# Kernel tuning notes

Hardware: AMD Instinct MI355X
Metric: run time of the kernel (lower is better)

Reference implementation:

```python
import jax, jax.numpy as jnp
import numpy as np

N_NODES = 2048
IN_FEAT = 128
N_HEADS = 4
N_HIDDEN = 16  # out_features // n_heads = 64 // 4
NEG_SLOPE = 0.2


def setup_inputs() -> dict:
    key = jax.random.key(0)
    k1, k2, k3, k4, k5 = jax.random.split(key, 5)
    h = jax.random.normal(k1, (N_NODES, IN_FEAT), dtype=jnp.float32)
    adj_mat = jax.random.randint(k2, (N_NODES, N_NODES, 1), 0, 2, dtype=jnp.int32)
    scale_w = 1.0 / np.sqrt(IN_FEAT)
    W_l = jax.random.normal(k3, (IN_FEAT, N_HEADS * N_HIDDEN), dtype=jnp.float32) * scale_w
    W_r = jax.random.normal(k4, (IN_FEAT, N_HEADS * N_HIDDEN), dtype=jnp.float32) * scale_w
    attn_w = jax.random.normal(k5, (N_HIDDEN,), dtype=jnp.float32) / np.sqrt(N_HIDDEN)
    return {"h": h, "adj_mat": adj_mat, "W_l": W_l, "W_r": W_r, "attn_w": attn_w}


def reference(h, adj_mat, W_l, W_r, attn_w):
    n = h.shape[0]
    g_l = (h @ W_l).reshape(n, N_HEADS, N_HIDDEN)  # source-side proj
    g_r = (h @ W_r).reshape(n, N_HEADS, N_HIDDEN)  # target-side proj
    # g_sum[i, j, h, f] = g_r[i] + g_l[j]  (matches repeat / repeat_interleave in torch)
    g_sum = g_r[:, None, :, :] + g_l[None, :, :, :]  # [N, N, H, F]
    e = jnp.einsum('ijhf,f->ijh', jax.nn.leaky_relu(g_sum, NEG_SLOPE), attn_w)
    e = jnp.where(adj_mat == 0, -jnp.inf, e)
    a = jnp.nan_to_num(jax.nn.softmax(e, axis=1))  # softmax over neighbors j
    attn_res = jnp.einsum('ijh,jhf->ihf', a, g_r)
    return attn_res.reshape(n, N_HEADS * N_HIDDEN)  # is_concat=True
```

## Files before the change

### kernel.cpp

```cpp
#include <hip/hip_runtime.h>
#include <math.h>
#include <stdint.h>

#define NN 2048
#define IF 128
#define NH 4
#define NF 16
#define OF 64
#define JS 2
#define JT 16
#define NPW 2
#define NPB 8
#define PSTR 17
#define LOG2E 1.44269504f


typedef float f32x2 __attribute__((ext_vector_type(2)));
typedef float f32x4 __attribute__((ext_vector_type(4)));

__device__ __forceinline__ float rfl(float x) {
    return __int_as_float(__builtin_amdgcn_readfirstlane(__float_as_int(x)));
}
__device__ __forceinline__ void gl2lds16(const void* g, void* l) {
    __builtin_amdgcn_global_load_lds((const __attribute__((address_space(1))) void*)g,
                                     (__attribute__((address_space(3))) void*)l, 16, 0, 0);
}
__device__ __forceinline__ void gl2lds4(const void* g, void* l) {
    __builtin_amdgcn_global_load_lds((const __attribute__((address_space(1))) void*)g,
                                     (__attribute__((address_space(3))) void*)l, 4, 0, 0);
}

__global__ __launch_bounds__(256) void pack_kernel(const int* __restrict__ adj,
                                                   uint32_t* __restrict__ bits) {
    const int w = threadIdx.x >> 6, lane = threadIdx.x & 63;
    const int i = blockIdx.x * 4 + w;
    const int* row = adj + (size_t)i * NN;
    uint64_t*  dst = (uint64_t*)bits + (size_t)i * 32;
    #pragma unroll 4
    for (int k = 0; k < 32; ++k) {
        const int v = row[k * 64 + lane];
        const uint64_t msk = __ballot(v != 0);
        if (lane == 0) dst[k] = msk;
    }
}

__global__ __launch_bounds__(256) void proj_kernel(const float* __restrict__ h,
                                                   const float* __restrict__ Wl,
                                                   const float* __restrict__ Wr,
                                                   const float* __restrict__ attn_w,
                                                   float* __restrict__ glt,
                                                   float* __restrict__ grt,
                                                   float* __restrict__ cj6,
                                                   float* __restrict__ cjB,
                                                   float* __restrict__ ai2) {
    const int t    = threadIdx.x;
    const int w    = t >> 6, lane = t & 63;
    const int il   = w >> 1, which = w & 1;
    const int i    = blockIdx.x * 2 + il;

    __shared__ float hs[2][IF];
    hs[t >> 7][t & 127] = h[(blockIdx.x * 2 + (t >> 7)) * IF + (t & 127)];
    __syncthreads();

    const float* W = which ? Wr : Wl;
    float acc = 0.f;
    #pragma unroll
    for (int k = 0; k < IF; ++k)
        acc = fmaf(hs[il][k], W[k * OF + lane], acc);

    float* g = which ? grt : glt;
    g[(lane >> 4) * (NN * NF) + i * NF + (lane & 15)] = acc;

    const float awv = attn_w[lane & 15];
    float v  = acc * awv;
    float vb = fabsf(acc) * fabsf(awv);
    #pragma unroll
    for (int off = 1; off <= 8; off <<= 1) {
        v  += __shfl_xor(v,  off);
        vb += __shfl_xor(vb, off);
    }
    if ((lane & 15) == 0) {
        const int hh = lane >> 4;
        if (which) {
            ai2[hh * NN + i] = 0.4f * LOG2E * vb;
        } else {
            const float c2 = 0.6f * LOG2E * v;
            cj6[hh * NN + i] = c2;
            cjB[hh * NN + i] = fmaf(0.4f * LOG2E, vb, c2);
        }
    }
}

__global__ __launch_bounds__(256) void mh_kernel(const float* __restrict__ cjB,
                                                 float* __restrict__ mh) {
    const int hh = blockIdx.x, t = threadIdx.x;
    float mx = -INFINITY;
    for (int j = t; j < NN; j += 256) mx = fmaxf(mx, cjB[hh * NN + j]);
    #pragma unroll
    for (int off = 32; off; off >>= 1) mx = fmaxf(mx, __shfl_xor(mx, off));
    __shared__ float wmx[4];
    if ((t & 63) == 0) wmx[t >> 6] = mx;
    __syncthreads();
    if (t == 0) mh[hh] = fmaxf(fmaxf(wmx[0], wmx[1]), fmaxf(wmx[2], wmx[3]));
}

__global__ __launch_bounds__(256) __attribute__((amdgpu_waves_per_eu(2, 8)))
void gat_kernel(const float* __restrict__ glt,
                const float* __restrict__ grt,
                const float* __restrict__ cj6,
                const float* __restrict__ ai2,
                const float* __restrict__ mh,
                const uint32_t* __restrict__ bits,
                const float* __restrict__ attn_w,
                float* __restrict__ part) {
    const int t    = threadIdx.x;
    const int wid  = t >> 6, lane = t & 63;
    const int h    = blockIdx.x & 3;
    const int grp  = (blockIdx.x >> 2) & 255;
    const int s    = blockIdx.x >> 10;

    __shared__ __attribute__((aligned(16))) char smem[17920];
    float*    tile   = (float*)smem;
    uint32_t* bits_s = (uint32_t*)(smem + 16384);
    float*    c_s    = (float*)(smem + 17408);

    {
        const int idx = wid * 64 + lane;
        gl2lds4(bits + ((size_t)(grp * 8 + (idx >> 5))) * 64 + s * 32 + (idx & 31),
                smem + 16384 + wid * 256);
    }

    float aw_s[NF];
    #pragma unroll
    for (int f = 0; f < NF; ++f) aw_s[f] = rfl(attn_w[f]) * (0.4f * LOG2E);
    const float mh_s = rfl(mh[h]);
    float gi_s[NPW][NF], cni[NPW];
    #pragma unroll
    for (int n = 0; n < NPW; ++n) {
        const int i_n = grp * NPB + wid * NPW + n;
        #pragma unroll
        for (int f = 0; f < NF; ++f)
            gi_s[n][f] = rfl(grt[h * (NN * NF) + i_n * NF + f]);
        cni[n] = -(rfl(ai2[h * NN + i_n]) + mh_s);
    }

    const float* glh = glt + (size_t)h * NN * NF + (size_t)s * JT * 64 * NF;
    const float* grh = grt + (size_t)h * NN * NF + (size_t)s * JT * 64 * NF;
    const float* cjh = cj6 + h * NN + s * (JT * 64);

    const int soff = (wid * 16 + (lane >> 2)) * NF + (((lane & 3) ^ ((lane >> 3) & 3)) << 2);

#define STAGE(tl, nb)                                                              \
    {                                                                              \
        gl2lds16(glh + (size_t)(tl) * (64 * NF) + soff, smem + (nb) * 4096 + wid * 1024);        \
        gl2lds16(grh + (size_t)(tl) * (64 * NF) + soff, smem + 8192 + (nb) * 4096 + wid * 1024); \
        if (wid == 0) gl2lds4(cjh + (tl) * 64 + lane, smem + 17408 + (nb) * 256);  \
    }

    float l[NPW];
    f32x2 acc[NPW][8];
    #pragma unroll
    for (int n = 0; n < NPW; ++n) {
        l[n] = 0.f;
        #pragma unroll
        for (int k = 0; k < 8; ++k) acc[n][k] = (f32x2){0.f, 0.f};
    }

    STAGE(0, 0);
    __syncthreads();

    const int sh   = lane & 31;
    const int csw  = (lane >> 1) & 3;
    #pragma unroll 2
    for (int tt = 0; tt < JT; ++tt) {
        const int buf = tt & 1;
        if (tt + 1 < JT) STAGE(tt + 1, buf ^ 1);

        float ss[NPW] = {0.f, 0.f};
        #pragma unroll
        for (int q = 0; q < 4; ++q) {
            const int c = q ^ csw;
            const f32x4 gv = *(const f32x4*)&tile[buf * 1024 + lane * NF + c * 4];
            #pragma unroll
            for (int n = 0; n < NPW; ++n) {
                ss[n] = fmaf(fabsf(gv[0] + gi_s[n][q * 4 + 0]), aw_s[q * 4 + 0], ss[n]);
                ss[n] = fmaf(fabsf(gv[1] + gi_s[n][q * 4 + 1]), aw_s[q * 4 + 1], ss[n]);
                ss[n] = fmaf(fabsf(gv[2] + gi_s[n][q * 4 + 2]), aw_s[q * 4 + 2], ss[n]);
                ss[n] = fmaf(fabsf(gv[3] + gi_s[n][q * 4 + 3]), aw_s[q * 4 + 3], ss[n]);
            }
        }
        const float cj = c_s[buf * 64 + lane];

        float p[NPW];
        #pragma unroll
        for (int n = 0; n < NPW; ++n) {
            const uint32_t wb = bits_s[(wid * NPW + n) * 32 + tt * 2 + (lane >> 5)];
            const bool  kk = ((wb >> sh) & 1u) != 0u;
            float e = (ss[n] + cj) + cni[n];
            e = kk ? e : -INFINITY;
            const float pp = __builtin_amdgcn_exp2f(e);
            l[n] += pp;
            p[n] = pp;
        }

        #pragma unroll
        for (int q = 0; q < 4; ++q) {
            const int c = q ^ csw;
            const f32x4 rv = *(const f32x4*)&tile[2048 + buf * 1024 + lane * NF + c * 4];
            const f32x2 lo = {rv[0], rv[1]};
            const f32x2 hi = {rv[2], rv[3]};
            #pragma unroll
            for (int n = 0; n < NPW; ++n) {
                const f32x2 pp2 = {p[n], p[n]};
                acc[n][q * 2 + 0] = __builtin_elementwise_fma(pp2, lo, acc[n][q * 2 + 0]);
                acc[n][q * 2 + 1] = __builtin_elementwise_fma(pp2, hi, acc[n][q * 2 + 1]);
            }
        }
        __syncthreads();
    }
#undef STAGE

    float (*red)[16][PSTR] = (float (*)[16][PSTR])smem;
    #pragma unroll
    for (int n = 0; n < NPW; ++n) {
        float L = l[n];
        #pragma unroll
        for (int off = 32; off; off >>= 1) L += __shfl_xor(L, off);

        #pragma unroll
        for (int f = 0; f < NF; ++f) {
            float a = acc[n][f >> 1][f & 1];
            a += __shfl_xor(a, 32);
            a += __shfl_xor(a, 16);
            if (lane < 16) red[wid][lane][f] = a;
        }
        const int i_n = grp * NPB + wid * NPW + n;
        float* P = part + ((size_t)s * NH * NN + (size_t)h * NN + i_n) * PSTR;
        if (lane < NF) {
            float a = 0.f;
            #pragma unroll
            for (int r = 0; r < 16; ++r) a += red[wid][r][lane];
            P[lane] = a;
        } else if (lane == 16) P[16] = L;
    }
}

__global__ __launch_bounds__(256) void reduce_kernel(const float* __restrict__ part,
                                                     float* __restrict__ out) {
    const int c  = blockIdx.x * 256 + threadIdx.x;
    const int f  = c & 15;
    const int ih = c >> 4;
    float L = 0.f, a = 0.f;
    #pragma unroll
    for (int ss = 0; ss < JS; ++ss) {
        const float* P = part + ((size_t)ss * NH * NN + ih) * PSTR;
        a += P[f];
        L += P[16];
    }
    const float o = (L > 0.f) ? a / L : 0.f;
    const int i = ih & (NN - 1);
    const int h = ih >> 11;
    out[(size_t)i * OF + h * NF + f] = o;
}

extern "C" void kernel_launch(void* const* d_in, const int* in_sizes, int n_in,
                              void* d_out, int out_size, void* d_ws, size_t ws_size,
                              hipStream_t stream) {
    const float* h      = (const float*)d_in[0];
    const int*   adj    = (const int*)d_in[1];
    const float* W_l    = (const float*)d_in[2];
    const float* W_r    = (const float*)d_in[3];
    const float* attn_w = (const float*)d_in[4];
    float*       out    = (float*)d_out;

    float*    glt  = (float*)d_ws;
    float*    grt  = glt + (size_t)NN * OF;
    float*    cj6  = grt + (size_t)NN * OF;
    float*    cjB  = cj6 + (size_t)NH * NN;
    float*    ai2  = cjB + (size_t)NH * NN;
    float*    mh   = ai2 + (size_t)NH * NN;
    uint32_t* bits = (uint32_t*)(mh + 64);
    float*    prt  = (float*)(bits + (size_t)NN * 64);

    pack_kernel<<<NN / 4, 256, 0, stream>>>(adj, bits);
    proj_kernel<<<NN / 2, 256, 0, stream>>>(h, W_l, W_r, attn_w, glt, grt, cj6, cjB, ai2);
    mh_kernel<<<NH, 256, 0, stream>>>(cjB, mh);
    gat_kernel<<<JS * 256 * NH, 256, 0, stream>>>(glt, grt, cj6, ai2, mh, bits, attn_w, prt);
    reduce_kernel<<<NH * NN * NF / 256, 256, 0, stream>>>(prt, out);
}
```

Measured before the change: 60.74 us.

## Load j-tiles directly into registers and double node count per wave

The attention kernel stops staging gl/gr tiles through LDS with a barrier per tile. Each lane now loads its own j-row straight from global memory into registers, double-buffered across two steps. Each wave also handles 4 target nodes instead of 2, so every loaded j-row is reused more and the grid shrinks to half as many blocks. The cost is much higher register pressure (waves_per_eu capped at 3), lower occupancy and fewer blocks to spread latency hiding.

```diff
diff --git a/kernel.cpp b/kernel.cpp
--- a/kernel.cpp
+++ b/kernel.cpp
@@ -9,21 +9,16 @@
 #define OF 64
 #define JS 2
 #define JT 16
-#define NPW 2
-#define NPB 8
+#define NPW 4
+#define NPB 16
 #define PSTR 17
 #define LOG2E 1.44269504f
 
-
 typedef float f32x2 __attribute__((ext_vector_type(2)));
 typedef float f32x4 __attribute__((ext_vector_type(4)));
 
 __device__ __forceinline__ float rfl(float x) {
     return __int_as_float(__builtin_amdgcn_readfirstlane(__float_as_int(x)));
-}
-__device__ __forceinline__ void gl2lds16(const void* g, void* l) {
-    __builtin_amdgcn_global_load_lds((const __attribute__((address_space(1))) void*)g,
-                                     (__attribute__((address_space(3))) void*)l, 16, 0, 0);
 }
 __device__ __forceinline__ void gl2lds4(const void* g, void* l) {
     __builtin_amdgcn_global_load_lds((const __attribute__((address_space(1))) void*)g,
@@ -104,7 +99,7 @@
     if (t == 0) mh[hh] = fmaxf(fmaxf(wmx[0], wmx[1]), fmaxf(wmx[2], wmx[3]));
 }
 
-__global__ __launch_bounds__(256) __attribute__((amdgpu_waves_per_eu(2, 8)))
+__global__ __launch_bounds__(256) __attribute__((amdgpu_waves_per_eu(2, 3)))
 void gat_kernel(const float* __restrict__ glt,
                 const float* __restrict__ grt,
                 const float* __restrict__ cj6,
@@ -116,18 +111,25 @@
     const int t    = threadIdx.x;
     const int wid  = t >> 6, lane = t & 63;
     const int h    = blockIdx.x & 3;
-    const int grp  = (blockIdx.x >> 2) & 255;
-    const int s    = blockIdx.x >> 10;
-
-    __shared__ __attribute__((aligned(16))) char smem[17920];
-    float*    tile   = (float*)smem;
-    uint32_t* bits_s = (uint32_t*)(smem + 16384);
-    float*    c_s    = (float*)(smem + 17408);
-
+    const int grp  = (blockIdx.x >> 2) & 127;
+    const int s    = blockIdx.x >> 9;
+
+    __shared__ uint32_t bits_s[NPB * 32];
+    __shared__ float    c_all[JT * 64];
+    __shared__ float    red[4][16][PSTR];
+
+    #pragma unroll
+    for (int k = 0; k < 2; ++k) {
+        const int f = wid * 128 + k * 64 + lane;
+        gl2lds4(bits + ((size_t)(grp * 16 + (f >> 5))) * 64 + s * 32 + (f & 31),
+                (char*)bits_s + (wid * 128 + k * 64) * 4);
+    }
     {
-        const int idx = wid * 64 + lane;
-        gl2lds4(bits + ((size_t)(grp * 8 + (idx >> 5))) * 64 + s * 32 + (idx & 31),
-                smem + 16384 + wid * 256);
+        const float* cjh = cj6 + h * NN + s * (JT * 64);
+        #pragma unroll
+        for (int k = 0; k < 4; ++k)
+            gl2lds4(cjh + k * 256 + wid * 64 + lane,
+                    (char*)c_all + (k * 256 + wid * 64) * 4);
     }
 
     float aw_s[NF];
@@ -144,17 +146,60 @@
         cni[n] = -(rfl(ai2[h * NN + i_n]) + mh_s);
     }
 
-    const float* glh = glt + (size_t)h * NN * NF + (size_t)s * JT * 64 * NF;
-    const float* grh = grt + (size_t)h * NN * NF + (size_t)s * JT * 64 * NF;
-    const float* cjh = cj6 + h * NN + s * (JT * 64);
-
-    const int soff = (wid * 16 + (lane >> 2)) * NF + (((lane & 3) ^ ((lane >> 3) & 3)) << 2);
-
-#define STAGE(tl, nb)                                                              \
-    {                                                                              \
-        gl2lds16(glh + (size_t)(tl) * (64 * NF) + soff, smem + (nb) * 4096 + wid * 1024);        \
-        gl2lds16(grh + (size_t)(tl) * (64 * NF) + soff, smem + 8192 + (nb) * 4096 + wid * 1024); \
-        if (wid == 0) gl2lds4(cjh + (tl) * 64 + lane, smem + 17408 + (nb) * 256);  \
+    const float* pg = glt + (size_t)h * NN * NF + (size_t)s * JT * 64 * NF + (size_t)lane * NF;
+    const float* pr = grt + (size_t)h * NN * NF + (size_t)s * JT * 64 * NF + (size_t)lane * NF;
+
+    __syncthreads();
+
+#define LOADG(tl, G)                                                      \
+    {                                                                     \
+        const float* b = pg + (size_t)(tl) * (64 * NF);                   \
+        G[0] = *(const f32x4*)(b);      G[1] = *(const f32x4*)(b + 4);    \
+        G[2] = *(const f32x4*)(b + 8);  G[3] = *(const f32x4*)(b + 12);   \
+    }
+#define LOADR(tl)                                                         \
+    {                                                                     \
+        const float* b = pr + (size_t)(tl) * (64 * NF);                   \
+        rC[0] = *(const f32x4*)(b);     rC[1] = *(const f32x4*)(b + 4);   \
+        rC[2] = *(const f32x4*)(b + 8); rC[3] = *(const f32x4*)(b + 12);  \
+    }
+#define STEP(G, tt)                                                       \
+    {                                                                     \
+        float ss[NPW] = {0.f, 0.f, 0.f, 0.f};                             \
+        _Pragma("unroll")                                                 \
+        for (int q = 0; q < 4; ++q) {                                     \
+            const f32x4 gv = G[q];                                        \
+            _Pragma("unroll")                                             \
+            for (int n = 0; n < NPW; ++n) {                               \
+                ss[n] = fmaf(fabsf(gv[0] + gi_s[n][q*4+0]), aw_s[q*4+0], ss[n]); \
+                ss[n] = fmaf(fabsf(gv[1] + gi_s[n][q*4+1]), aw_s[q*4+1], ss[n]); \
+                ss[n] = fmaf(fabsf(gv[2] + gi_s[n][q*4+2]), aw_s[q*4+2], ss[n]); \
+                ss[n] = fmaf(fabsf(gv[3] + gi_s[n][q*4+3]), aw_s[q*4+3], ss[n]); \
+            }                                                             \
+        }                                                                 \
+        const float cj = c_all[(tt) * 64 + lane];                         \
+        float p[NPW];                                                     \
+        _Pragma("unroll")                                                 \
+        for (int n = 0; n < NPW; ++n) {                                   \
+            const uint32_t wb = bits_s[(wid*NPW+n)*32 + (tt)*2 + (lane>>5)]; \
+            const bool  kk = ((wb >> sh) & 1u) != 0u;                     \
+            float e = (ss[n] + cj) + cni[n];                              \
+            e = kk ? e : -INFINITY;                                       \
+            const float pp = __builtin_amdgcn_exp2f(e);                   \
+            l[n] += pp;                                                   \
+            p[n] = pp;                                                    \
+        }                                                                 \
+        _Pragma("unroll")                                                 \
+        for (int q = 0; q < 4; ++q) {                                     \
+            const f32x2 lo = {rC[q][0], rC[q][1]};                        \
+            const f32x2 hi = {rC[q][2], rC[q][3]};                        \
+            _Pragma("unroll")                                             \
+            for (int n = 0; n < NPW; ++n) {                               \
+                const f32x2 pp2 = {p[n], p[n]};                           \
+                acc[n][q*2+0] = __builtin_elementwise_fma(pp2, lo, acc[n][q*2+0]); \
+                acc[n][q*2+1] = __builtin_elementwise_fma(pp2, hi, acc[n][q*2+1]); \
+            }                                                             \
+        }                                                                 \
     }
 
     float l[NPW];
@@ -166,61 +211,22 @@
         for (int k = 0; k < 8; ++k) acc[n][k] = (f32x2){0.f, 0.f};
     }
 
-    STAGE(0, 0);
-    __syncthreads();
-
-    const int sh   = lane & 31;
-    const int csw  = (lane >> 1) & 3;
-    #pragma unroll 2
-    for (int tt = 0; tt < JT; ++tt) {
-        const int buf = tt & 1;
-        if (tt + 1 < JT) STAGE(tt + 1, buf ^ 1);
-
-        float ss[NPW] = {0.f, 0.f};
-        #pragma unroll
-        for (int q = 0; q < 4; ++q) {
-            const int c = q ^ csw;
-            const f32x4 gv = *(const f32x4*)&tile[buf * 1024 + lane * NF + c * 4];
-            #pragma unroll
-            for (int n = 0; n < NPW; ++n) {
-                ss[n] = fmaf(fabsf(gv[0] + gi_s[n][q * 4 + 0]), aw_s[q * 4 + 0], ss[n]);
-                ss[n] = fmaf(fabsf(gv[1] + gi_s[n][q * 4 + 1]), aw_s[q * 4 + 1], ss[n]);
-                ss[n] = fmaf(fabsf(gv[2] + gi_s[n][q * 4 + 2]), aw_s[q * 4 + 2], ss[n]);
-                ss[n] = fmaf(fabsf(gv[3] + gi_s[n][q * 4 + 3]), aw_s[q * 4 + 3], ss[n]);
-            }
-        }
-        const float cj = c_s[buf * 64 + lane];
-
-        float p[NPW];
-        #pragma unroll
-        for (int n = 0; n < NPW; ++n) {
-            const uint32_t wb = bits_s[(wid * NPW + n) * 32 + tt * 2 + (lane >> 5)];
-            const bool  kk = ((wb >> sh) & 1u) != 0u;
-            float e = (ss[n] + cj) + cni[n];
-            e = kk ? e : -INFINITY;
-            const float pp = __builtin_amdgcn_exp2f(e);
-            l[n] += pp;
-            p[n] = pp;
-        }
-
-        #pragma unroll
-        for (int q = 0; q < 4; ++q) {
-            const int c = q ^ csw;
-            const f32x4 rv = *(const f32x4*)&tile[2048 + buf * 1024 + lane * NF + c * 4];
-            const f32x2 lo = {rv[0], rv[1]};
-            const f32x2 hi = {rv[2], rv[3]};
-            #pragma unroll
-            for (int n = 0; n < NPW; ++n) {
-                const f32x2 pp2 = {p[n], p[n]};
-                acc[n][q * 2 + 0] = __builtin_elementwise_fma(pp2, lo, acc[n][q * 2 + 0]);
-                acc[n][q * 2 + 1] = __builtin_elementwise_fma(pp2, hi, acc[n][q * 2 + 1]);
-            }
-        }
-        __syncthreads();
-    }
-#undef STAGE
-
-    float (*red)[16][PSTR] = (float (*)[16][PSTR])smem;
+    const int sh = lane & 31;
+    f32x4 gA[4], gB[4], rC[4];
+
+    LOADG(0, gA);
+    for (int tt = 0; tt < JT; tt += 2) {
+        LOADR(tt);
+        LOADG(tt + 1, gB);
+        STEP(gA, tt);
+        LOADR(tt + 1);
+        if (tt + 2 < JT) LOADG(tt + 2, gA);
+        STEP(gB, tt + 1);
+    }
+#undef LOADG
+#undef LOADR
+#undef STEP
+
     #pragma unroll
     for (int n = 0; n < NPW; ++n) {
         float L = l[n];
@@ -285,6 +291,6 @@
     pack_kernel<<<NN / 4, 256, 0, stream>>>(adj, bits);
     proj_kernel<<<NN / 2, 256, 0, stream>>>(h, W_l, W_r, attn_w, glt, grt, cj6, cjB, ai2);
     mh_kernel<<<NH, 256, 0, stream>>>(cjB, mh);
-    gat_kernel<<<JS * 256 * NH, 256, 0, stream>>>(glt, grt, cj6, ai2, mh, bits, attn_w, prt);
+    gat_kernel<<<JS * 128 * NH, 256, 0, stream>>>(glt, grt, cj6, ai2, mh, bits, attn_w, prt);
     reduce_kernel<<<NH * NN * NF / 256, 256, 0, stream>>>(prt, out);
 }
```

Result: slower. 66.68 us (+9.8%).
